# Kernel optimization log

Measured on AMD Instinct MI355X. Metric: run time of the kernel, lower is better.

The kernel has to match this reference:

```python
import jax, jax.numpy as jnp
import numpy as np

B, S, C, H = 8, 512, 512, 8
E_MOD, E_SH, K = 4, 2, 2
E = E_MOD + E_SH          # total experts routed over
D = C // H                # head dim
RH = max(int(C * 1), C)   # router hidden (mlp_ratio=1)
EPS = 1e-8


def setup_inputs() -> dict:
    key = jax.random.key(0)
    ks = jax.random.split(key, 12)
    s = 0.02
    x = jax.random.normal(ks[0], (B, S, C), jnp.float32)
    mask = jax.random.randint(ks[1], (B, 3 * S), 0, 2).astype(bool)

    def w(k, shape):
        return jax.random.normal(k, shape, jnp.float32) * s

    return dict(
        x=x, mask=mask,
        qw=w(ks[2], (E, C, C)), qb=jnp.zeros((E, C), jnp.float32),
        kw=w(ks[3], (E, C, C)), kb=jnp.zeros((E, C), jnp.float32),
        vw=w(ks[4], (E, C, C)), vb=jnp.zeros((E, C), jnp.float32),
        fc1w=w(ks[5], (E, C, C)), fc1b=jnp.zeros((E, C), jnp.float32),
        fc2w=w(ks[6], (E, C, C)), fc2b=jnp.zeros((E, C), jnp.float32),
        rw1=w(ks[7], (C, RH)), rb1=jnp.zeros((RH,), jnp.float32),
        rw2=w(ks[8], (RH, E)), rb2=jnp.zeros((E,), jnp.float32),
    )


def _experts(x, mask_a, qw, qb, kw, kb, vw, vb, fc1w, fc1b, fc2w, fc2b):
    # All E Attention experts, vectorized over expert axis e.
    scale = D ** (-0.5)

    def proj(w, b):
        t = jnp.einsum('bsc,ecd->ebsd', x, w) + b[:, None, None, :]
        return t.reshape(E, B, S, H, D).transpose(0, 1, 3, 2, 4)  # [E,B,H,S,D]

    q = proj(qw, qb) * scale
    k = proj(kw, kb)
    v = proj(vw, vb)
    # fp32 scores, masked softmax over keys, nan-sanitization (fully masked rows -> 0)
    attn = jnp.einsum('ebhsd,ebhtd->ebhst', q.astype(jnp.float32), k.astype(jnp.float32))
    attn = jnp.where(mask_a[None, :, None, None, :], attn, -jnp.inf)
    attn = jax.nn.softmax(attn, axis=-1).astype(x.dtype)
    attn = jnp.where(jnp.isnan(attn), jnp.zeros((), x.dtype), attn)
    xo = jnp.einsum('ebhst,ebhtd->ebhsd', attn, v)
    xo = xo.transpose(0, 1, 3, 2, 4).reshape(E, B, S, C)
    # residual Mlp (exact GELU, dropout=0)
    h = jax.nn.gelu(jnp.einsum('ebsc,ecd->ebsd', xo, fc1w) + fc1b[:, None, None, :], approximate=False)
    xo = xo + jnp.einsum('ebsd,edc->ebsc', h, fc2w) + fc2b[:, None, None, :]
    return xo  # [E,B,S,C]


def reference(x, mask, qw, qb, kw, kb, vw, vb, fc1w, fc1b, fc2w, fc2b, rw1, rb1, rw2, rb2):
    mask_a = mask[:, :S]  # mask_modality='a'
    xo = _experts(x, mask_a, qw, qb, kw, kb, vw, vb, fc1w, fc1b, fc2w, fc2b)
    stacked = xo.transpose(1, 2, 0, 3)  # [B,S,E,C]

    # Router Mlp: fc1 -> GELU -> fc2 (eval mode, no noise)
    rh = jax.nn.gelu(jnp.einsum('bsc,ch->bsh', x, rw1) + rb1, approximate=False)
    logits = jnp.einsum('bsh,he->bse', rh, rw2) + rb2
    rwts = jax.nn.softmax(logits, axis=-1)  # [B,S,E]

    # top-k masking + renormalization
    top_vals, top_idx = jax.lax.top_k(rwts, K)
    sparse = jnp.sum(top_vals[..., None] * jax.nn.one_hot(top_idx, E, dtype=rwts.dtype), axis=-2)
    sparse = sparse / jnp.maximum(sparse.sum(axis=-1, keepdims=True), EPS)

    aggregated = jnp.einsum('bse,bsec->bsc', sparse, stacked)
    return aggregated, stacked, sparse
```

## Files before the change

kernel.cpp:

```cpp
#include <hip/hip_runtime.h>

typedef unsigned short u16;
typedef unsigned int   u32;
typedef unsigned long long u64;
typedef __bf16 bf16x8 __attribute__((ext_vector_type(8)));
typedef float  f32x4  __attribute__((ext_vector_type(4)));

#define NE    6
#define MTOT  4096
#define CC    512
#define BMAT  262144
#define EMAT  2097152

#define FLAG_OFF 0
#define XBF_OFF  256
#define WT_OFF   (XBF_OFF + MTOT*CC*2)
#define QBF_OFF  (WT_OFF  + 30*BMAT*2)
#define KBF_OFF  (QBF_OFF + NE*EMAT*2)
#define VT_OFF   (KBF_OFF + NE*EMAT*2)
#define XO_OFF   (VT_OFF  + NE*EMAT*2)
#define HBF_OFF  (XO_OFF  + NE*EMAT*2)
#define RH_OFF   (HBF_OFF + NE*EMAT*2)

__device__ __forceinline__ u16 f2bf(float f) {
    u32 u = __float_as_uint(f);
    u32 r = (u + 0x7FFFu + ((u >> 16) & 1u)) >> 16;
    return (u16)r;
}
__device__ __forceinline__ u16 f2bf_hw(float f) {
    __bf16 h = (__bf16)f;
    return *(u16*)&h;
}
__device__ __forceinline__ float bf2f(u16 h) {
    return __uint_as_float(((u32)h) << 16);
}
__device__ __forceinline__ u32 cvt_pk_bf16(float a, float b) {
    u32 r;
    asm("v_cvt_pk_bf16_f32 %0, %1, %2" : "=v"(r) : "v"(a), "v"(b));
    return r;
}
__device__ __forceinline__ float gelu_exact(float x) {
    return 0.5f * x * (1.0f + erff(x * 0.70710678118654752f));
}
__device__ __forceinline__ bool mask_valid(const void* mask, int flag, int b, int t) {
    int idx = b * 1536 + t;
    if (flag == 1) return ((const int*)mask)[idx] != 0;
    if (flag == 2) return ((const float*)mask)[idx] != 0.0f;
    return ((const unsigned char*)mask)[idx] != 0;
}

__global__ void detect_mask_k(const u32* __restrict__ m, int* __restrict__ flag) {
    __shared__ int notint, notfloat;
    if (threadIdx.x == 0) { notint = 0; notfloat = 0; }
    __syncthreads();
    int ni = 0, nf = 0;
    for (int i = threadIdx.x; i < 3072; i += 256) {
        u32 v = m[i];
        if (v > 1u) ni = 1;
        if (v != 0u && v != 0x3F800000u) nf = 1;
    }
    if (ni) notint = 1;
    if (nf) notfloat = 1;
    __syncthreads();
    if (threadIdx.x == 0) *flag = (notint == 0) ? 1 : ((notfloat == 0) ? 2 : 0);
}

__global__ __launch_bounds__(256) void cast_x_k(const float* __restrict__ x, u16* __restrict__ xbf) {
    int i = blockIdx.x * 256 + threadIdx.x;
    float4 v = ((const float4*)x)[i];
    u64 pk = (u64)f2bf(v.x) | ((u64)f2bf(v.y) << 16) | ((u64)f2bf(v.z) << 32) | ((u64)f2bf(v.w) << 48);
    *(u64*)(xbf + (size_t)i * 4) = pk;
}

__global__ __launch_bounds__(256) void transpose_w_k(
    const float* __restrict__ qw, const float* __restrict__ kw, const float* __restrict__ vw,
    const float* __restrict__ f1w, const float* __restrict__ f2w, u16* __restrict__ wt) {
    int mat = blockIdx.y;
    int tile = blockIdx.x;
    int tr = tile >> 4, tc = tile & 15;
    const float* srcs[5] = {qw, kw, vw, f1w, f2w};
    const float* src = srcs[mat / 6] + (size_t)(mat % 6) * BMAT;
    u16* dst = wt + (size_t)mat * BMAT;
    __shared__ float tb[32][33];
    int r = threadIdx.x >> 5, c = threadIdx.x & 31;
    #pragma unroll
    for (int i = 0; i < 4; ++i)
        tb[r + i * 8][c] = src[(size_t)(tr * 32 + r + i * 8) * CC + tc * 32 + c];
    __syncthreads();
    #pragma unroll
    for (int i = 0; i < 4; ++i)
        dst[(size_t)(tc * 32 + r + i * 8) * CC + tr * 32 + c] = f2bf(tb[c][r + i * 8]);
}

__global__ __launch_bounds__(256) void router_rh_k(
    const float* __restrict__ x, const float* __restrict__ rw1, const float* __restrict__ rb1,
    float* __restrict__ rh) {
    const int n0 = blockIdx.x * 64, m0 = blockIdx.y * 64;
    const int tid = threadIdx.x, tx = tid & 15, ty = tid >> 4;
    __shared__ float As[64][20];
    __shared__ float Bs[16][68];
    float acc[4][4] = {};
    for (int kt = 0; kt < 32; ++kt) {
        int ar = tid >> 2, ak = (tid & 3) * 4;
        float4 av = *(const float4*)(x + (size_t)(m0 + ar) * CC + kt * 16 + ak);
        int br = tid >> 4, bn = (tid & 15) * 4;
        float4 bv = *(const float4*)(rw1 + (size_t)(kt * 16 + br) * CC + n0 + bn);
        __syncthreads();
        *(float4*)&As[ar][ak] = av;
        *(float4*)&Bs[br][bn] = bv;
        __syncthreads();
        #pragma unroll
        for (int k = 0; k < 16; ++k) {
            float a[4], b[4];
            #pragma unroll
            for (int i = 0; i < 4; ++i) a[i] = As[ty * 4 + i][k];
            #pragma unroll
            for (int j = 0; j < 4; ++j) b[j] = Bs[k][tx * 4 + j];
            #pragma unroll
            for (int i = 0; i < 4; ++i)
                #pragma unroll
                for (int j = 0; j < 4; ++j) acc[i][j] = fmaf(a[i], b[j], acc[i][j]);
        }
    }
    #pragma unroll
    for (int i = 0; i < 4; ++i) {
        int m = m0 + ty * 4 + i;
        #pragma unroll
        for (int j = 0; j < 4; ++j) {
            int n = n0 + tx * 4 + j;
            rh[(size_t)m * CC + n] = gelu_exact(acc[i][j] + rb1[n]);
        }
    }
}

__global__ __launch_bounds__(256) void router_topk_k(
    const float* __restrict__ rh, const float* __restrict__ rw2, const float* __restrict__ rb2,
    float* __restrict__ sparse) {
    int row = blockIdx.x * 4 + (threadIdx.x >> 6);
    int lane = threadIdx.x & 63;
    float acc[NE] = {};
    const float* rr = rh + (size_t)row * CC;
    for (int c = 0; c < 8; ++c) {
        int k = c * 64 + lane;
        float v = rr[k];
        const float* w = rw2 + (size_t)k * NE;
        #pragma unroll
        for (int e = 0; e < NE; ++e) acc[e] = fmaf(v, w[e], acc[e]);
    }
    #pragma unroll
    for (int off = 32; off; off >>= 1)
        #pragma unroll
        for (int e = 0; e < NE; ++e) acc[e] += __shfl_down(acc[e], off);
    if (lane == 0) {
        float lg[NE], m = -1e30f;
        #pragma unroll
        for (int e = 0; e < NE; ++e) { lg[e] = acc[e] + rb2[e]; m = fmaxf(m, lg[e]); }
        float s = 0.f, wv[NE];
        #pragma unroll
        for (int e = 0; e < NE; ++e) { wv[e] = expf(lg[e] - m); s += wv[e]; }
        #pragma unroll
        for (int e = 0; e < NE; ++e) wv[e] /= s;
        int i1 = 0; float v1 = wv[0];
        #pragma unroll
        for (int e = 1; e < NE; ++e) if (wv[e] > v1) { v1 = wv[e]; i1 = e; }
        int i2 = -1; float v2 = -1.f;
        #pragma unroll
        for (int e = 0; e < NE; ++e) if (e != i1 && wv[e] > v2) { v2 = wv[e]; i2 = e; }
        float denom = fmaxf(v1 + v2, 1e-8f);
        #pragma unroll
        for (int e = 0; e < NE; ++e)
            sparse[(size_t)row * NE + e] = ((e == i1) ? v1 : (e == i2) ? v2 : 0.f) / denom;
    }
}

template<int MODE>
__global__ __launch_bounds__(256, 3) void gemm_k(
    const u16* __restrict__ A0, const u16* __restrict__ wt,
    u16* __restrict__ out_bf, float* __restrict__ out_f32,
    const u16* __restrict__ resid, const float* __restrict__ bias0) {
    const int e = blockIdx.z;
    const u16* A  = (MODE <= 2) ? A0 : (A0 + (size_t)e * EMAT);
    const int wmat = (MODE == 0 ? 0 : MODE == 1 ? 6 : MODE == 2 ? 12 : MODE == 3 ? 18 : 24) + e;
    const u16* BT = wt + (size_t)wmat * BMAT;
    const float* bias = bias0 + e * CC;

    const int m0 = blockIdx.y * 128, n0 = blockIdx.x * 128;
    const int tid = threadIdx.x, lane = tid & 63, wv = tid >> 6;
    const int l15 = lane & 15, quad = lane >> 4;
    const int wr = (wv >> 1) * 64, wc = (wv & 1) * 64;

    __shared__ u16 As[128 * 40];
    __shared__ u16 Bs[128 * 40];

    f32x4 acc[4][4];
    f32x4 z4 = {0.f, 0.f, 0.f, 0.f};
    #pragma unroll
    for (int i = 0; i < 4; ++i)
        #pragma unroll
        for (int j = 0; j < 4; ++j) acc[i][j] = z4;

    const int row2 = tid >> 1, half = tid & 1;
    const u16* agp = A  + (size_t)(m0 + row2) * CC + half * 16;
    const u16* bgp = BT + (size_t)(n0 + row2) * CC + half * 16;
    u16* asp = As + row2 * 40 + half * 16;
    u16* bsp = Bs + row2 * 40 + half * 16;

    for (int kt = 0; kt < 16; ++kt) {
        uint4 a0 = *(const uint4*)(agp + kt * 32);
        uint4 a1 = *(const uint4*)(agp + kt * 32 + 8);
        uint4 b0 = *(const uint4*)(bgp + kt * 32);
        uint4 b1 = *(const uint4*)(bgp + kt * 32 + 8);
        __syncthreads();
        *(uint4*)asp = a0; *(uint4*)(asp + 8) = a1;
        *(uint4*)bsp = b0; *(uint4*)(bsp + 8) = b1;
        __syncthreads();
        bf16x8 af[4], bf[4];
        #pragma unroll
        for (int i = 0; i < 4; ++i) af[i] = *(const bf16x8*)(As + (wr + i * 16 + l15) * 40 + quad * 8);
        #pragma unroll
        for (int j = 0; j < 4; ++j) bf[j] = *(const bf16x8*)(Bs + (wc + j * 16 + l15) * 40 + quad * 8);
        #pragma unroll
        for (int i = 0; i < 4; ++i)
            #pragma unroll
            for (int j = 0; j < 4; ++j)
                acc[i][j] = __builtin_amdgcn_mfma_f32_16x16x32_bf16(af[i], bf[j], acc[i][j], 0, 0, 0);
    }

    #pragma unroll
    for (int i = 0; i < 4; ++i) {
        int mb = m0 + wr + i * 16 + quad * 4;
        #pragma unroll
        for (int j = 0; j < 4; ++j) {
            int n = n0 + wc + j * 16 + l15;
            float bvs = bias[n];
            if (MODE == 2) {
                u16 pk[4];
                #pragma unroll
                for (int r = 0; r < 4; ++r) pk[r] = f2bf(acc[i][j][r] + bvs);
                u64 w8 = (u64)pk[0] | ((u64)pk[1] << 16) | ((u64)pk[2] << 32) | ((u64)pk[3] << 48);
                *(u64*)(out_bf + (size_t)e * EMAT + (size_t)n * MTOT + mb) = w8;
            } else if (MODE == 0 || MODE == 1) {
                #pragma unroll
                for (int r = 0; r < 4; ++r) {
                    float v = acc[i][j][r] + bvs;
                    out_bf[(size_t)e * EMAT + (size_t)(mb + r) * CC + n] =
                        f2bf(MODE == 0 ? v * 0.18033688011112042f : v);
                }
            } else if (MODE == 3) {
                #pragma unroll
                for (int r = 0; r < 4; ++r)
                    out_bf[(size_t)e * EMAT + (size_t)(mb + r) * CC + n] = f2bf(gelu_exact(acc[i][j][r] + bvs));
            } else {
                #pragma unroll
                for (int r = 0; r < 4; ++r) {
                    int m = mb + r;
                    float v = acc[i][j][r] + bvs + bf2f(resid[(size_t)e * EMAT + (size_t)m * CC + n]);
                    out_f32[((size_t)m * NE + e) * CC + n] = v;
                }
            }
        }
    }
}

__global__ __launch_bounds__(256, 3) void attn_flash_k(
    const u16* __restrict__ qbf, const u16* __restrict__ kbf, const u16* __restrict__ vt,
    u16* __restrict__ xobf, const void* __restrict__ mask, const int* __restrict__ flagp) {
    const int b = blockIdx.y >> 3, h = blockIdx.y & 7;
    const int e = blockIdx.z;
    const int tid = threadIdx.x, lane = tid & 63, w = tid >> 6;
    const int l15 = lane & 15, quad = lane >> 4;
    const int s0 = blockIdx.x * 256 + w * 64;
    const int flag = *flagp;

    __shared__ float mlds[512];
    mlds[tid]       = mask_valid(mask, flag, b, tid)       ? 1.f : 0.f;
    mlds[tid + 256] = mask_valid(mask, flag, b, tid + 256) ? 1.f : 0.f;
    __syncthreads();

    const u16* qbase = qbf + (size_t)e * EMAT + (size_t)(b * 512) * CC + h * 64;
    const u16* kbase = kbf + (size_t)e * EMAT + (size_t)(b * 512) * CC + h * 64;
    const u16* vbase = vt  + (size_t)e * EMAT + (size_t)(h * 64) * MTOT + b * 512;

    bf16x8 qa[4][2];
    #pragma unroll
    for (int t = 0; t < 4; ++t) {
        qa[t][0] = *(const bf16x8*)(qbase + (size_t)(s0 + t * 16 + l15) * CC + quad * 8);
        qa[t][1] = *(const bf16x8*)(qbase + (size_t)(s0 + t * 16 + l15) * CC + 32 + quad * 8);
    }

    float lsum[4] = {0.f, 0.f, 0.f, 0.f};
    f32x4 o[4][4];
    f32x4 z4 = {0.f, 0.f, 0.f, 0.f};
    #pragma unroll
    for (int t = 0; t < 4; ++t)
        #pragma unroll
        for (int j = 0; j < 4; ++j) o[t][j] = z4;

    for (int ch = 0; ch < 16; ++ch) {
        const int k0 = ch * 32;
        bf16x8 kb00 = *(const bf16x8*)(kbase + (size_t)(k0 + l15) * CC + quad * 8);
        bf16x8 kb01 = *(const bf16x8*)(kbase + (size_t)(k0 + l15) * CC + 32 + quad * 8);
        bf16x8 kb10 = *(const bf16x8*)(kbase + (size_t)(k0 + 16 + l15) * CC + quad * 8);
        bf16x8 kb11 = *(const bf16x8*)(kbase + (size_t)(k0 + 16 + l15) * CC + 32 + quad * 8);
        bf16x8 vf[4];
        #pragma unroll
        for (int j = 0; j < 4; ++j) {
            const u16* vr = vbase + (size_t)(j * 16 + l15) * MTOT + k0 + quad * 4;
            uint2 lo = *(const uint2*)(vr);
            uint2 hi = *(const uint2*)(vr + 16);
            union { u32 u[4]; bf16x8 v; } vv;
            vv.u[0] = lo.x; vv.u[1] = lo.y; vv.u[2] = hi.x; vv.u[3] = hi.y;
            vf[j] = vv.v;
        }
        float4 m0v = *(const float4*)(mlds + k0 + quad * 4);
        float4 m1v = *(const float4*)(mlds + k0 + 16 + quad * 4);

        #pragma unroll
        for (int t = 0; t < 4; ++t) {
            f32x4 c0 = z4, c1 = z4;
            c0 = __builtin_amdgcn_mfma_f32_16x16x32_bf16(kb00, qa[t][0], c0, 0, 0, 0);
            c0 = __builtin_amdgcn_mfma_f32_16x16x32_bf16(kb01, qa[t][1], c0, 0, 0, 0);
            c1 = __builtin_amdgcn_mfma_f32_16x16x32_bf16(kb10, qa[t][0], c1, 0, 0, 0);
            c1 = __builtin_amdgcn_mfma_f32_16x16x32_bf16(kb11, qa[t][1], c1, 0, 0, 0);
            float p0[4], p1[4];
            p0[0] = exp2f(c0[0]) * m0v.x;  p0[1] = exp2f(c0[1]) * m0v.y;
            p0[2] = exp2f(c0[2]) * m0v.z;  p0[3] = exp2f(c0[3]) * m0v.w;
            p1[0] = exp2f(c1[0]) * m1v.x;  p1[1] = exp2f(c1[1]) * m1v.y;
            p1[2] = exp2f(c1[2]) * m1v.z;  p1[3] = exp2f(c1[3]) * m1v.w;
            lsum[t] += ((p0[0] + p0[1]) + (p0[2] + p0[3]))
                     + ((p1[0] + p1[1]) + (p1[2] + p1[3]));
            union { u32 u[4]; bf16x8 v; } pp;
            pp.u[0] = cvt_pk_bf16(p0[0], p0[1]);
            pp.u[1] = cvt_pk_bf16(p0[2], p0[3]);
            pp.u[2] = cvt_pk_bf16(p1[0], p1[1]);
            pp.u[3] = cvt_pk_bf16(p1[2], p1[3]);
            #pragma unroll
            for (int j = 0; j < 4; ++j)
                o[t][j] = __builtin_amdgcn_mfma_f32_16x16x32_bf16(pp.v, vf[j], o[t][j], 0, 0, 0);
        }
    }

    #pragma unroll
    for (int t = 0; t < 4; ++t) {
        float l = lsum[t];
        l += __shfl_xor(l, 16);
        l += __shfl_xor(l, 32);
        #pragma unroll
        for (int r = 0; r < 4; ++r) {
            float lv = __shfl(l, quad * 4 + r);
            float inv = (lv > 0.f) ? 1.f / lv : 0.f;
            int row = s0 + t * 16 + quad * 4 + r;
            u16* xb = xobf + (size_t)e * EMAT + (size_t)(b * 512 + row) * CC + h * 64;
            #pragma unroll
            for (int j = 0; j < 4; ++j)
                xb[j * 16 + l15] = f2bf_hw(o[t][j][r] * inv);
        }
    }
}

__global__ __launch_bounds__(256) void aggregate_k(
    const float* __restrict__ stacked, const float* __restrict__ sparse, float* __restrict__ agg) {
    int idx = blockIdx.x * 256 + threadIdx.x;
    int m = idx >> 7;
    int c4 = (idx & 127) << 2;
    const float* sp = sparse + (size_t)m * NE;
    float4 a = {0.f, 0.f, 0.f, 0.f};
    #pragma unroll
    for (int e = 0; e < NE; ++e) {
        float s = sp[e];
        float4 v = *(const float4*)(stacked + ((size_t)m * NE + e) * CC + c4);
        a.x = fmaf(s, v.x, a.x); a.y = fmaf(s, v.y, a.y);
        a.z = fmaf(s, v.z, a.z); a.w = fmaf(s, v.w, a.w);
    }
    ((float4*)agg)[idx] = a;
}

extern "C" void kernel_launch(void* const* d_in, const int* in_sizes, int n_in,
                              void* d_out, int out_size, void* d_ws, size_t ws_size,
                              hipStream_t stream) {
    const float* x   = (const float*)d_in[0];
    const void*  mask = d_in[1];
    const float* qw = (const float*)d_in[2];   const float* qb = (const float*)d_in[3];
    const float* kw = (const float*)d_in[4];   const float* kb = (const float*)d_in[5];
    const float* vw = (const float*)d_in[6];   const float* vb = (const float*)d_in[7];
    const float* f1w = (const float*)d_in[8];  const float* f1b = (const float*)d_in[9];
    const float* f2w = (const float*)d_in[10]; const float* f2b = (const float*)d_in[11];
    const float* rw1 = (const float*)d_in[12]; const float* rb1 = (const float*)d_in[13];
    const float* rw2 = (const float*)d_in[14]; const float* rb2 = (const float*)d_in[15];

    float* out = (float*)d_out;
    float* agg     = out;
    float* stacked = out + 2097152;
    float* sparse  = out + 14680064;

    char* ws = (char*)d_ws;
    int* flag = (int*)(ws + FLAG_OFF);
    u16* xbf = (u16*)(ws + XBF_OFF);
    u16* wt  = (u16*)(ws + WT_OFF);
    u16* qbf = (u16*)(ws + QBF_OFF);
    u16* kbf = (u16*)(ws + KBF_OFF);
    u16* vt  = (u16*)(ws + VT_OFF);
    u16* xob = (u16*)(ws + XO_OFF);
    u16* hbf = (u16*)(ws + HBF_OFF);
    float* rh = (float*)(ws + RH_OFF);

    detect_mask_k<<<1, 256, 0, stream>>>((const u32*)mask, flag);
    cast_x_k<<<2048, 256, 0, stream>>>(x, xbf);
    transpose_w_k<<<dim3(256, 30), 256, 0, stream>>>(qw, kw, vw, f1w, f2w, wt);
    router_rh_k<<<dim3(8, 64), 256, 0, stream>>>(x, rw1, rb1, rh);
    router_topk_k<<<1024, 256, 0, stream>>>(rh, rw2, rb2, sparse);

    dim3 gg(4, 32, 6);
    gemm_k<0><<<gg, 256, 0, stream>>>(xbf, wt, qbf, nullptr, nullptr, qb);
    gemm_k<1><<<gg, 256, 0, stream>>>(xbf, wt, kbf, nullptr, nullptr, kb);
    gemm_k<2><<<gg, 256, 0, stream>>>(xbf, wt, vt,  nullptr, nullptr, vb);
    attn_flash_k<<<dim3(2, 64, 6), 256, 0, stream>>>(qbf, kbf, vt, xob, mask, flag);
    gemm_k<3><<<gg, 256, 0, stream>>>(xob, wt, hbf, nullptr, nullptr, f1b);
    gemm_k<4><<<gg, 256, 0, stream>>>(hbf, wt, nullptr, stacked, xob, f2b);
    aggregate_k<<<2048, 256, 0, stream>>>(stacked, sparse, agg);
}
```

Measured before the change: 400.0 us.

## Prefetch K/V fragments, permute V^T layout for 16-byte loads, use native exp2

The V-projection epilogue now writes transposed V with a permuted column order, so the attention kernel can load each V fragment with a single 16-byte load instead of two 8-byte loads. The attention loop is fully unrolled and double-buffers the K fragments, loading the next chunk's K before the current compute and V after it, to hide global-load latency. It also switches exp2f to the native hardware exp2 builtin and uses compiler bf16 casts instead of inline asm. The costs are higher register pressure, which could lower occupancy, and slightly different exp2 and rounding behaviour.

```diff
diff --git a/kernel.cpp b/kernel.cpp
--- a/kernel.cpp
+++ b/kernel.cpp
@@ -34,10 +34,12 @@
 __device__ __forceinline__ float bf2f(u16 h) {
     return __uint_as_float(((u32)h) << 16);
 }
-__device__ __forceinline__ u32 cvt_pk_bf16(float a, float b) {
-    u32 r;
-    asm("v_cvt_pk_bf16_f32 %0, %1, %2" : "=v"(r) : "v"(a), "v"(b));
-    return r;
+__device__ __forceinline__ float exp2_native(float x) {
+#if __has_builtin(__builtin_amdgcn_exp2f)
+    return __builtin_amdgcn_exp2f(x);
+#else
+    return exp2f(x);
+#endif
 }
 __device__ __forceinline__ float gelu_exact(float x) {
     return 0.5f * x * (1.0f + erff(x * 0.70710678118654752f));
@@ -238,7 +240,8 @@
                 #pragma unroll
                 for (int r = 0; r < 4; ++r) pk[r] = f2bf(acc[i][j][r] + bvs);
                 u64 w8 = (u64)pk[0] | ((u64)pk[1] << 16) | ((u64)pk[2] << 32) | ((u64)pk[3] << 48);
-                *(u64*)(out_bf + (size_t)e * EMAT + (size_t)n * MTOT + mb) = w8;
+                int mp = (mb & ~31) | (((mb >> 2) & 3) << 3) | (((mb >> 4) & 1) << 2);
+                *(u64*)(out_bf + (size_t)e * EMAT + (size_t)n * MTOT + mp) = w8;
             } else if (MODE == 0 || MODE == 1) {
                 #pragma unroll
                 for (int r = 0; r < 4; ++r) {
@@ -296,47 +299,58 @@
         #pragma unroll
         for (int j = 0; j < 4; ++j) o[t][j] = z4;
 
+    bf16x8 kf[2][4], vf[4];
+    kf[0][0] = *(const bf16x8*)(kbase + (size_t)(l15) * CC + quad * 8);
+    kf[0][1] = *(const bf16x8*)(kbase + (size_t)(l15) * CC + 32 + quad * 8);
+    kf[0][2] = *(const bf16x8*)(kbase + (size_t)(16 + l15) * CC + quad * 8);
+    kf[0][3] = *(const bf16x8*)(kbase + (size_t)(16 + l15) * CC + 32 + quad * 8);
+    #pragma unroll
+    for (int j = 0; j < 4; ++j)
+        vf[j] = *(const bf16x8*)(vbase + (size_t)(j * 16 + l15) * MTOT + quad * 8);
+
+    #pragma unroll
     for (int ch = 0; ch < 16; ++ch) {
-        const int k0 = ch * 32;
-        bf16x8 kb00 = *(const bf16x8*)(kbase + (size_t)(k0 + l15) * CC + quad * 8);
-        bf16x8 kb01 = *(const bf16x8*)(kbase + (size_t)(k0 + l15) * CC + 32 + quad * 8);
-        bf16x8 kb10 = *(const bf16x8*)(kbase + (size_t)(k0 + 16 + l15) * CC + quad * 8);
-        bf16x8 kb11 = *(const bf16x8*)(kbase + (size_t)(k0 + 16 + l15) * CC + 32 + quad * 8);
-        bf16x8 vf[4];
-        #pragma unroll
-        for (int j = 0; j < 4; ++j) {
-            const u16* vr = vbase + (size_t)(j * 16 + l15) * MTOT + k0 + quad * 4;
-            uint2 lo = *(const uint2*)(vr);
-            uint2 hi = *(const uint2*)(vr + 16);
-            union { u32 u[4]; bf16x8 v; } vv;
-            vv.u[0] = lo.x; vv.u[1] = lo.y; vv.u[2] = hi.x; vv.u[3] = hi.y;
-            vf[j] = vv.v;
-        }
+        const int cur = ch & 1, nxt = cur ^ 1;
+        const int k0 = ch * 32, kn = k0 + 32;
+
+        if (ch < 15) {
+            kf[nxt][0] = *(const bf16x8*)(kbase + (size_t)(kn + l15) * CC + quad * 8);
+            kf[nxt][1] = *(const bf16x8*)(kbase + (size_t)(kn + l15) * CC + 32 + quad * 8);
+            kf[nxt][2] = *(const bf16x8*)(kbase + (size_t)(kn + 16 + l15) * CC + quad * 8);
+            kf[nxt][3] = *(const bf16x8*)(kbase + (size_t)(kn + 16 + l15) * CC + 32 + quad * 8);
+        }
+
         float4 m0v = *(const float4*)(mlds + k0 + quad * 4);
         float4 m1v = *(const float4*)(mlds + k0 + 16 + quad * 4);
 
         #pragma unroll
         for (int t = 0; t < 4; ++t) {
             f32x4 c0 = z4, c1 = z4;
-            c0 = __builtin_amdgcn_mfma_f32_16x16x32_bf16(kb00, qa[t][0], c0, 0, 0, 0);
-            c0 = __builtin_amdgcn_mfma_f32_16x16x32_bf16(kb01, qa[t][1], c0, 0, 0, 0);
-            c1 = __builtin_amdgcn_mfma_f32_16x16x32_bf16(kb10, qa[t][0], c1, 0, 0, 0);
-            c1 = __builtin_amdgcn_mfma_f32_16x16x32_bf16(kb11, qa[t][1], c1, 0, 0, 0);
+            c0 = __builtin_amdgcn_mfma_f32_16x16x32_bf16(kf[cur][0], qa[t][0], c0, 0, 0, 0);
+            c0 = __builtin_amdgcn_mfma_f32_16x16x32_bf16(kf[cur][1], qa[t][1], c0, 0, 0, 0);
+            c1 = __builtin_amdgcn_mfma_f32_16x16x32_bf16(kf[cur][2], qa[t][0], c1, 0, 0, 0);
+            c1 = __builtin_amdgcn_mfma_f32_16x16x32_bf16(kf[cur][3], qa[t][1], c1, 0, 0, 0);
             float p0[4], p1[4];
-            p0[0] = exp2f(c0[0]) * m0v.x;  p0[1] = exp2f(c0[1]) * m0v.y;
-            p0[2] = exp2f(c0[2]) * m0v.z;  p0[3] = exp2f(c0[3]) * m0v.w;
-            p1[0] = exp2f(c1[0]) * m1v.x;  p1[1] = exp2f(c1[1]) * m1v.y;
-            p1[2] = exp2f(c1[2]) * m1v.z;  p1[3] = exp2f(c1[3]) * m1v.w;
+            p0[0] = exp2_native(c0[0]) * m0v.x;  p0[1] = exp2_native(c0[1]) * m0v.y;
+            p0[2] = exp2_native(c0[2]) * m0v.z;  p0[3] = exp2_native(c0[3]) * m0v.w;
+            p1[0] = exp2_native(c1[0]) * m1v.x;  p1[1] = exp2_native(c1[1]) * m1v.y;
+            p1[2] = exp2_native(c1[2]) * m1v.z;  p1[3] = exp2_native(c1[3]) * m1v.w;
             lsum[t] += ((p0[0] + p0[1]) + (p0[2] + p0[3]))
                      + ((p1[0] + p1[1]) + (p1[2] + p1[3]));
-            union { u32 u[4]; bf16x8 v; } pp;
-            pp.u[0] = cvt_pk_bf16(p0[0], p0[1]);
-            pp.u[1] = cvt_pk_bf16(p0[2], p0[3]);
-            pp.u[2] = cvt_pk_bf16(p1[0], p1[1]);
-            pp.u[3] = cvt_pk_bf16(p1[2], p1[3]);
+            union { __bf16 hh[8]; bf16x8 v; } pp;
+            pp.hh[0] = (__bf16)p0[0]; pp.hh[1] = (__bf16)p0[1];
+            pp.hh[2] = (__bf16)p0[2]; pp.hh[3] = (__bf16)p0[3];
+            pp.hh[4] = (__bf16)p1[0]; pp.hh[5] = (__bf16)p1[1];
+            pp.hh[6] = (__bf16)p1[2]; pp.hh[7] = (__bf16)p1[3];
             #pragma unroll
             for (int j = 0; j < 4; ++j)
                 o[t][j] = __builtin_amdgcn_mfma_f32_16x16x32_bf16(pp.v, vf[j], o[t][j], 0, 0, 0);
+        }
+
+        if (ch < 15) {
+            #pragma unroll
+            for (int j = 0; j < 4; ++j)
+                vf[j] = *(const bf16x8*)(vbase + (size_t)(j * 16 + l15) * MTOT + kn + quad * 8);
         }
     }
 
```

After: 795.2 us. +98.8%, slower.
